# Kernel tuning notes

Hardware: AMD Instinct MI355X
Metric: run time of the kernel (lower is better)

## Reference

```python
import jax, jax.numpy as jnp
import numpy as np

B, T, D_MODEL = 2, 1024, 512
EXPAND = 2
D_INNER = D_MODEL * EXPAND
STATE = 16
K_CONV = 4


def setup_inputs() -> dict:
    key = jax.random.key(0)
    ks = jax.random.split(key, 10)
    sc = lambda k, shape: jax.random.normal(k, shape, jnp.float32) * 0.02
    return {
        "x": jax.random.normal(ks[0], (B, T, D_MODEL), jnp.float32),
        "ln_g": jnp.ones((D_MODEL,), jnp.float32),
        "ln_b": jnp.zeros((D_MODEL,), jnp.float32),
        "W_in": sc(ks[1], (2 * D_INNER, D_MODEL)),
        "conv_w": sc(ks[2], (D_INNER, 1, K_CONV)),
        "conv_b": jnp.zeros((D_INNER,), jnp.float32),
        "W_B": sc(ks[3], (STATE, D_INNER)),
        "W_C": sc(ks[4], (STATE, D_INNER)),
        "W_dt": sc(ks[5], (D_INNER, D_INNER)),
        "b_dt": jax.random.uniform(ks[6], (D_INNER,), jnp.float32, -4.0, -1.0),
        # log_A init: A_diag = -(n+1) from HiPPO, log(-A_diag) = log(n+1), broadcast over d_inner
        "log_A": jnp.broadcast_to(jnp.log(jnp.arange(1, STATE + 1, dtype=jnp.float32)), (D_INNER, STATE)),
        "W_out": sc(ks[7], (D_MODEL, D_INNER)),
    }


def _silu(v):
    return v * jax.nn.sigmoid(v)


def reference(x, ln_g, ln_b, W_in, conv_w, conv_b, W_B, W_C, W_dt, b_dt, log_A, W_out):
    residual = x
    # LayerNorm (biased variance, eps=1e-5)
    mu = x.mean(-1, keepdims=True)
    var = x.var(-1, keepdims=True)
    xn = (x - mu) * jax.lax.rsqrt(var + 1e-5) * ln_g + ln_b
    # input projection and gate split
    xz = xn @ W_in.T                      # (B,T,2*D_INNER)
    x_main, z = jnp.split(xz, 2, axis=-1)
    # depthwise causal conv1d (padding=3 then slice to T == left-pad 3)
    xc = jnp.transpose(x_main, (0, 2, 1))  # (B,D_INNER,T)
    xc = jax.lax.conv_general_dilated(
        xc, conv_w, window_strides=(1,), padding=[(K_CONV - 1, 0)],
        dimension_numbers=("NCH", "OIH", "NCH"), feature_group_count=D_INNER,
    ) + conv_b[None, :, None]
    x_main = _silu(jnp.transpose(xc, (0, 2, 1)))  # (B,T,D_INNER)
    # selective scan in fp32
    xf = x_main.astype(jnp.float32)
    Bt = xf @ W_B.T                        # (B,T,N)
    Ct = xf @ W_C.T                        # (B,T,N)
    dt = jax.nn.softplus(xf @ W_dt.T + b_dt)  # (B,T,D_INNER)
    A = -jnp.exp(log_A)                    # (D_INNER,N)
    dA = jnp.exp(A[None, None] * dt[..., None])              # (B,T,D_INNER,N)
    dBx = dt[..., None] * Bt[:, :, None, :] * xf[..., None]  # (B,T,D_INNER,N)

    def comb(c1, c2):
        a1, b1 = c1
        a2, b2 = c2
        return a1 * a2, a2 * b1 + b2

    _, h = jax.lax.associative_scan(comb, (dA, dBx), axis=1)  # h_t = dA_t*h_{t-1}+dBx_t
    y = (h * Ct[:, :, None, :]).sum(-1).astype(x.dtype)       # (B,T,D_INNER)
    out = (y * _silu(z)) @ W_out.T
    return residual + out
```

## Files before the change

kernel.cpp:

```cpp
#include <hip/hip_runtime.h>

#define T_SEQ 1024
#define DM 512
#define DI 1024
#define NS 16
#define NC 32
#define CL 32

typedef __attribute__((ext_vector_type(8))) short short8;
typedef __attribute__((ext_vector_type(4))) float f32x4;
typedef unsigned short u16;
typedef unsigned int u32;

__device__ inline float b2f(u16 u) {
    unsigned v = ((unsigned)u) << 16;
    return __builtin_bit_cast(float, v);
}
__device__ inline u16 f2b(float f) {
    unsigned u = __builtin_bit_cast(unsigned, f);
    u += 0x7fff + ((u >> 16) & 1);
    return (u16)(u >> 16);
}

__device__ inline void g2l16(const u16* g, const short* l) {
    __builtin_amdgcn_global_load_lds((const __attribute__((address_space(1))) u32*)g,
                                     (__attribute__((address_space(3))) u32*)l, 16, 0, 0);
}

template<int K> __device__ __forceinline__ void vmwait() {
    if constexpr (K == 0) asm volatile("s_waitcnt vmcnt(0)" ::: "memory");
    else if constexpr (K == 2) asm volatile("s_waitcnt vmcnt(2)" ::: "memory");
}

__global__ __launch_bounds__(256) void prep_k(const float* __restrict__ Win, const float* __restrict__ Wdt,
                       const float* __restrict__ Wout, const float* __restrict__ Wb,
                       const float* __restrict__ Wc,
                       u16* __restrict__ oWin, u16* __restrict__ wCat, u16* __restrict__ oWout,
                       const float* __restrict__ x, const float* __restrict__ g,
                       const float* __restrict__ be, u16* __restrict__ xn) {
    if (blockIdx.x < 2624) {
        int i = blockIdx.x * 256 + threadIdx.x;
        const float* s; u16* d; int off;
        if (i < 262144)      { s = Win;  d = oWin;  off = i; }
        else if (i < 524288) { s = Wdt;  d = wCat;  off = i - 262144; }
        else if (i < 655360) { s = Wout; d = oWout; off = i - 524288; }
        else if (i < 659456) { s = Wb;   d = wCat + 1048576; off = i - 655360; }
        else if (i < 663552) { s = Wc;   d = wCat + 1064960; off = i - 659456; }
        else {
            u16* dz = wCat + 1081344 + (i - 663552) * 4;
            dz[0] = 0; dz[1] = 0; dz[2] = 0; dz[3] = 0;
            return;
        }
        float4 v = ((const float4*)s)[off];
        d[off * 4 + 0] = f2b(v.x);
        d[off * 4 + 1] = f2b(v.y);
        d[off * 4 + 2] = f2b(v.z);
        d[off * 4 + 3] = f2b(v.w);
        return;
    }
    int row = blockIdx.x - 2624, tid = threadIdx.x;
    float2 v = ((const float2*)(x + row * DM))[tid];
    float s = v.x + v.y, q = v.x * v.x + v.y * v.y;
    #pragma unroll
    for (int m = 1; m < 64; m <<= 1) { s += __shfl_xor(s, m); q += __shfl_xor(q, m); }
    __shared__ float ss[4], qq[4];
    if ((tid & 63) == 0) { ss[tid >> 6] = s; qq[tid >> 6] = q; }
    __syncthreads();
    s = ss[0] + ss[1] + ss[2] + ss[3];
    q = qq[0] + qq[1] + qq[2] + qq[3];
    float mu = s / DM;
    float var = q / DM - mu * mu;
    float rs = rsqrtf(var + 1e-5f);
    int c = tid * 2;
    xn[row * DM + c]     = f2b((v.x - mu) * rs * g[c] + be[c]);
    xn[row * DM + c + 1] = f2b((v.y - mu) * rs * g[c + 1] + be[c + 1]);
}

template<int NT, int EPI>
__device__ __forceinline__ void gemm_core64(int bx, int by,
        const u16* __restrict__ A, int lda, const u16* __restrict__ Bw, int ldb,
        void* __restrict__ outp, int ldo, const float* __restrict__ extra,
        float* __restrict__ BtF, float* __restrict__ CtF) {
    __shared__ short a_sh[3 * 4096];
    __shared__ short b_sh[3 * 4096];
    int tid = threadIdx.x, w = tid >> 6, lane = tid & 63;
    int m0 = bx * 64, n0 = by * 64;
    int wr = (w >> 2) * 32, wc = (w & 3) * 16;
    int lr = lane & 15, kg = lane >> 4;
    f32x4 acc[2] = {};
    const u16* Abase = A + (size_t)m0 * lda;
    const u16* Bbase = Bw + (size_t)n0 * ldb;
    int lrow = lane >> 3;
    int cl = lane & 7;
    int row1 = w * 8 + lrow;
    int sc = cl ^ (row1 & 7);

    auto stage = [&](int buf, int kt) {
        int k0 = kt * 64;
        g2l16(Abase + (size_t)row1 * lda + k0 + sc * 8, a_sh + buf * 4096 + w * 512);
        g2l16(Bbase + (size_t)row1 * ldb + k0 + sc * 8, b_sh + buf * 4096 + w * 512);
    };

    stage(0, 0);
    stage(1, 1);
    for (int t = 0; t < NT; ++t) {
        if (t + 1 < NT) vmwait<2>();
        else vmwait<0>();
        __builtin_amdgcn_s_barrier();
        if (t + 2 < NT) stage((t + 2) % 3, t + 2);
        const short* as = a_sh + (t % 3) * 4096;
        const short* bs = b_sh + (t % 3) * 4096;
        int rsw = lr & 7;
        __builtin_amdgcn_s_setprio(1);
        #pragma unroll
        for (int kk = 0; kk < 2; ++kk) {
            short8 af[2], bfr;
            #pragma unroll
            for (int i = 0; i < 2; ++i) {
                int row = wr + i * 16 + lr;
                af[i] = *(const short8*)&as[row * 64 + ((kk * 4 + kg) ^ rsw) * 8];
            }
            {
                int row = wc + lr;
                bfr = *(const short8*)&bs[row * 64 + ((kk * 4 + kg) ^ rsw) * 8];
            }
            #pragma unroll
            for (int i = 0; i < 2; ++i)
                acc[i] = __builtin_amdgcn_mfma_f32_16x16x32_bf16(af[i], bfr, acc[i], 0, 0, 0);
        }
        __builtin_amdgcn_s_setprio(0);
    }

    int rb = (lane >> 4) * 4, cc = lane & 15;
    #pragma unroll
    for (int i = 0; i < 2; ++i) {
        #pragma unroll
        for (int r = 0; r < 4; ++r) {
            int row = m0 + wr + i * 16 + rb + r;
            int col = n0 + wc + cc;
            float v = acc[i][r];
            if (EPI == 0) {
                ((u16*)outp)[(size_t)row * ldo + col] = f2b(v);
            } else if (EPI == 2) {
                ((float*)outp)[(size_t)row * ldo + col] = v + extra[(size_t)row * ldo + col];
            } else if (EPI == 3) {
                ((float*)outp)[(size_t)row * ldo + col] = v;
            } else {
                if (col < 1024) {
                    float xx = v + extra[col];
                    float sp = (xx > 20.f) ? xx : log1pf(__expf(xx));
                    ((u16*)outp)[(size_t)row * ldo + col] = f2b(sp);
                } else if (col < 1040) {
                    BtF[(size_t)row * NS + (col - 1024)] = v;
                } else if (col < 1056) {
                    CtF[(size_t)row * NS + (col - 1040)] = v;
                }
            }
        }
    }
}

template<int NT, int EPI>
__global__ __launch_bounds__(512) void gemm8(int gx,
                                             const u16* __restrict__ A, int lda,
                                             const u16* __restrict__ Bw, int ldb,
                                             void* __restrict__ outp, int ldo,
                                             const float* __restrict__ extra,
                                             float* __restrict__ BtF, float* __restrict__ CtF) {
    int bx = blockIdx.x % gx, by = blockIdx.x / gx;
    gemm_core64<NT, EPI>(bx, by, A, lda, Bw, ldb, outp, ldo, extra, BtF, CtF);
}

__global__ __launch_bounds__(512) void gemm2_k(const u16* __restrict__ ym, const u16* __restrict__ Wout,
                                               float* __restrict__ p0, float* __restrict__ p1) {
    int bid = blockIdx.x;
    int ks = bid >> 8, rem = bid & 255;
    int bx = rem & 31, by = rem >> 5;
    float* p = ks ? p1 : p0;
    gemm_core64<8, 3>(bx, by, ym + ks * 512, DI, Wout + ks * 512, DI,
                      (void*)p, DM, nullptr, nullptr, nullptr);
}

__global__ __launch_bounds__(256) void merge_k(const float* __restrict__ p0, const float* __restrict__ p1,
                                               const float* __restrict__ x, float* __restrict__ out) {
    int i = blockIdx.x * 256 + threadIdx.x;
    float4 a = ((const float4*)p0)[i];
    float4 b = ((const float4*)p1)[i];
    float4 e = ((const float4*)x)[i];
    float4 o;
    o.x = a.x + b.x + e.x;
    o.y = a.y + b.y + e.y;
    o.z = a.z + b.z + e.z;
    o.w = a.w + b.w + e.w;
    ((float4*)out)[i] = o;
}

__global__ void conv_k(const u16* __restrict__ xz, const float* __restrict__ w,
                       const float* __restrict__ cb, u16* __restrict__ xf) {
    int idx = blockIdx.x * 256 + threadIdx.x;
    int d = idx & (DI - 1);
    int bt = idx >> 10;
    int t = bt & (T_SEQ - 1);
    float s = cb[d];
    #pragma unroll
    for (int i = 0; i < 4; ++i) {
        int tt = t - 3 + i;
        if (tt >= 0) s += w[d * 4 + i] * b2f(xz[(size_t)(bt - 3 + i) * 2048 + d]);
    }
    float sig = 1.f / (1.f + __expf(-s));
    xf[idx] = f2b(s * sig);
}

__global__ __launch_bounds__(256) void scanA(const u16* __restrict__ dt, const u16* __restrict__ xf,
                                             const float* __restrict__ Bt, const float* __restrict__ logA,
                                             float* __restrict__ Aprod, float* __restrict__ S) {
    int tid = threadIdx.x;
    int dblk = blockIdx.x & 3;
    int c = (blockIdx.x >> 2) & (NC - 1);
    int b = blockIdx.x >> 7;
    int d = dblk * 256 + tid;
    float Adn[NS], ap[NS], h[NS];
    #pragma unroll
    for (int j = 0; j < 4; ++j)
        *(float4*)&Adn[j * 4] = ((const float4*)(logA + (size_t)d * NS))[j];
    #pragma unroll
    for (int n = 0; n < NS; ++n) { Adn[n] = -__expf(Adn[n]); ap[n] = 1.f; h[n] = 0.f; }
    const u16* dtp = dt + ((size_t)b * T_SEQ + c * CL) * DI + d;
    const u16* xfp = xf + ((size_t)b * T_SEQ + c * CL) * DI + d;
    const float* Bp = Bt + ((size_t)b * T_SEQ + c * CL) * NS;
    #pragma unroll 8
    for (int i = 0; i < CL; ++i) {
        float dtv = b2f(dtp[(size_t)i * DI]);
        float xv  = b2f(xfp[(size_t)i * DI]);
        float ux = dtv * xv;
        float Bv[NS];
        #pragma unroll
        for (int j = 0; j < 4; ++j) *(float4*)&Bv[j * 4] = ((const float4*)(Bp + (size_t)i * NS))[j];
        #pragma unroll
        for (int n = 0; n < NS; ++n) {
            float dA = __expf(Adn[n] * dtv);
            h[n] = fmaf(dA, h[n], ux * Bv[n]);
            ap[n] *= dA;
        }
    }
    size_t o = ((((size_t)c * 2 + b) * DI) + d) * NS;
    #pragma unroll
    for (int j = 0; j < 4; ++j) {
        ((float4*)(Aprod + o))[j] = *(float4*)&ap[j * 4];
        ((float4*)(S + o))[j]     = *(float4*)&h[j * 4];
    }
}

__global__ __launch_bounds__(256) void scanB(const float* __restrict__ Aprod, const float* __restrict__ S,
                                             float* __restrict__ Hin) {
    int chain = blockIdx.x * 256 + threadIdx.x;
    float h = 0.f;
    #pragma unroll 8
    for (int c = 0; c < NC; ++c) {
        size_t o = (size_t)c * 32768 + chain;
        Hin[o] = h;
        h = fmaf(Aprod[o], h, S[o]);
    }
}

__global__ __launch_bounds__(256) void scanC(const u16* __restrict__ dt, const u16* __restrict__ xf,
                                             const float* __restrict__ Bt, const float* __restrict__ Ct,
                                             const float* __restrict__ logA, const float* __restrict__ Hin,
                                             const u16* __restrict__ xz, u16* __restrict__ ym) {
    int tid = threadIdx.x;
    int dblk = blockIdx.x & 3;
    int c = (blockIdx.x >> 2) & (NC - 1);
    int b = blockIdx.x >> 7;
    int d = dblk * 256 + tid;
    float Adn[NS], h[NS];
    #pragma unroll
    for (int j = 0; j < 4; ++j)
        *(float4*)&Adn[j * 4] = ((const float4*)(logA + (size_t)d * NS))[j];
    #pragma unroll
    for (int n = 0; n < NS; ++n) Adn[n] = -__expf(Adn[n]);
    size_t o = ((((size_t)c * 2 + b) * DI) + d) * NS;
    #pragma unroll
    for (int j = 0; j < 4; ++j) *(float4*)&h[j * 4] = ((const float4*)(Hin + o))[j];
    const u16* dtp = dt + ((size_t)b * T_SEQ + c * CL) * DI + d;
    const u16* xfp = xf + ((size_t)b * T_SEQ + c * CL) * DI + d;
    const float* Bp = Bt + ((size_t)b * T_SEQ + c * CL) * NS;
    const float* Cp = Ct + ((size_t)b * T_SEQ + c * CL) * NS;
    const u16* zp = xz + ((size_t)b * T_SEQ + c * CL) * 2048 + 1024 + d;
    u16* yp = ym + ((size_t)b * T_SEQ + c * CL) * DI + d;
    #pragma unroll 8
    for (int i = 0; i < CL; ++i) {
        float dtv = b2f(dtp[(size_t)i * DI]);
        float xv  = b2f(xfp[(size_t)i * DI]);
        float ux = dtv * xv;
        float Bv[NS], Cv[NS];
        #pragma unroll
        for (int j = 0; j < 4; ++j) {
            *(float4*)&Bv[j * 4] = ((const float4*)(Bp + (size_t)i * NS))[j];
            *(float4*)&Cv[j * 4] = ((const float4*)(Cp + (size_t)i * NS))[j];
        }
        float r = 0.f;
        #pragma unroll
        for (int n = 0; n < NS; ++n) {
            float dA = __expf(Adn[n] * dtv);
            h[n] = fmaf(dA, h[n], ux * Bv[n]);
            r = fmaf(h[n], Cv[n], r);
        }
        float zv = b2f(zp[(size_t)i * 2048]);
        float sz = zv / (1.f + __expf(-zv));
        yp[(size_t)i * DI] = f2b(r * sz);
    }
}

extern "C" void kernel_launch(void* const* d_in, const int* in_sizes, int n_in,
                              void* d_out, int out_size, void* d_ws, size_t ws_size,
                              hipStream_t stream) {
    const float* x     = (const float*)d_in[0];
    const float* ln_g  = (const float*)d_in[1];
    const float* ln_b  = (const float*)d_in[2];
    const float* W_in  = (const float*)d_in[3];
    const float* conv_w= (const float*)d_in[4];
    const float* conv_b= (const float*)d_in[5];
    const float* W_B   = (const float*)d_in[6];
    const float* W_C   = (const float*)d_in[7];
    const float* W_dt  = (const float*)d_in[8];
    const float* b_dt  = (const float*)d_in[9];
    const float* log_A = (const float*)d_in[10];
    const float* W_out = (const float*)d_in[11];

    char* ws = (char*)d_ws;
    u16* wInB  = (u16*)(ws + 0);
    u16* wCat  = (u16*)(ws + 2097152);
    u16* wOutB = (u16*)(ws + 4325376);
    u16* xnB   = (u16*)(ws + 5373952);
    u16* xzB   = (u16*)(ws + 7471104);
    u16* xfB   = (u16*)(ws + 15859712);
    u16* dtB   = (u16*)(ws + 20054016);
    float* BtF = (float*)(ws + 24248320);
    float* CtF = (float*)(ws + 24379392);
    u16* ymB   = (u16*)(ws + 24510464);
    float* ApF = (float*)(ws + 28704768);
    float* SF  = (float*)(ws + 32899072);
    float* HiF = (float*)(ws + 37093376);

    prep_k<<<4672, 256, 0, stream>>>(W_in, W_dt, W_out, W_B, W_C, wInB, wCat, wOutB,
                                     x, ln_g, ln_b, xnB);
    gemm8<8, 0><<<1024, 512, 0, stream>>>(32, xnB, 512, wInB, 512,
            (void*)xzB, 2048, nullptr, nullptr, nullptr);
    conv_k<<<8192, 256, 0, stream>>>(xzB, conv_w, conv_b, xfB);
    gemm8<16, 4><<<544, 512, 0, stream>>>(32, xfB, 1024, wCat, 1024,
            (void*)dtB, 1024, b_dt, BtF, CtF);
    scanA<<<256, 256, 0, stream>>>(dtB, xfB, BtF, log_A, ApF, SF);
    scanB<<<128, 256, 0, stream>>>(ApF, SF, HiF);
    scanC<<<256, 256, 0, stream>>>(dtB, xfB, BtF, CtF, log_A, HiF, xzB, ymB);
    gemm2_k<<<512, 512, 0, stream>>>(ymB, wOutB, ApF, SF);
    merge_k<<<1024, 256, 0, stream>>>(ApF, SF, x, (float*)d_out);
}
```

Before: 112.7 us.

## Fuse three scan phases into one cooperative kernel and vectorize conv

The chunked scan's three kernels (local chunk scan, cross-chunk carry propagation, final output pass) are merged into one cooperative kernel with grid-wide syncs between phases. This removes two launches and their gaps, and keeps the per-thread A values resident across phases. Separately, the depthwise conv now processes four channels per thread with vector loads and stores, cutting the grid by a factor of four. The cooperative launch needs all 256 blocks co-resident, and grid.sync has its own barrier cost.

Result: slower. 175.6 us (+55.7%).

```diff
diff --git a/kernel.cpp b/kernel.cpp
--- a/kernel.cpp
+++ b/kernel.cpp
@@ -1,4 +1,7 @@
 #include <hip/hip_runtime.h>
+#include <hip/hip_cooperative_groups.h>
+
+namespace cg = cooperative_groups;
 
 #define T_SEQ 1024
 #define DM 512
@@ -195,119 +198,134 @@
     ((float4*)out)[i] = o;
 }
 
-__global__ void conv_k(const u16* __restrict__ xz, const float* __restrict__ w,
-                       const float* __restrict__ cb, u16* __restrict__ xf) {
-    int idx = blockIdx.x * 256 + threadIdx.x;
-    int d = idx & (DI - 1);
-    int bt = idx >> 10;
+__global__ __launch_bounds__(256) void conv_k(const u16* __restrict__ xz, const float* __restrict__ w,
+                                              const float* __restrict__ cb, u16* __restrict__ xf) {
+    int base = (blockIdx.x * 256 + threadIdx.x) * 4;
+    int d0 = base & (DI - 1);
+    int bt = base >> 10;
     int t = bt & (T_SEQ - 1);
-    float s = cb[d];
+    float4 cbv = *(const float4*)(cb + d0);
+    float s0 = cbv.x, s1 = cbv.y, s2 = cbv.z, s3 = cbv.w;
+    float4 w0 = *(const float4*)(w + (d0 + 0) * 4);
+    float4 w1 = *(const float4*)(w + (d0 + 1) * 4);
+    float4 w2 = *(const float4*)(w + (d0 + 2) * 4);
+    float4 w3 = *(const float4*)(w + (d0 + 3) * 4);
+    const float* pw0 = (const float*)&w0;
+    const float* pw1 = (const float*)&w1;
+    const float* pw2 = (const float*)&w2;
+    const float* pw3 = (const float*)&w3;
     #pragma unroll
     for (int i = 0; i < 4; ++i) {
         int tt = t - 3 + i;
-        if (tt >= 0) s += w[d * 4 + i] * b2f(xz[(size_t)(bt - 3 + i) * 2048 + d]);
-    }
-    float sig = 1.f / (1.f + __expf(-s));
-    xf[idx] = f2b(s * sig);
-}
-
-__global__ __launch_bounds__(256) void scanA(const u16* __restrict__ dt, const u16* __restrict__ xf,
-                                             const float* __restrict__ Bt, const float* __restrict__ logA,
-                                             float* __restrict__ Aprod, float* __restrict__ S) {
+        if (tt >= 0) {
+            ushort4 xv = *(const ushort4*)(xz + (size_t)(bt - 3 + i) * 2048 + d0);
+            s0 += pw0[i] * b2f(xv.x);
+            s1 += pw1[i] * b2f(xv.y);
+            s2 += pw2[i] * b2f(xv.z);
+            s3 += pw3[i] * b2f(xv.w);
+        }
+    }
+    ushort4 o;
+    o.x = f2b(s0 / (1.f + __expf(-s0)));
+    o.y = f2b(s1 / (1.f + __expf(-s1)));
+    o.z = f2b(s2 / (1.f + __expf(-s2)));
+    o.w = f2b(s3 / (1.f + __expf(-s3)));
+    *(ushort4*)(xf + base) = o;
+}
+
+__global__ __launch_bounds__(256) void scan_fused(const u16* __restrict__ dt, const u16* __restrict__ xf,
+                                                  const float* __restrict__ Bt, const float* __restrict__ Ct,
+                                                  const float* __restrict__ logA, const u16* __restrict__ xz,
+                                                  u16* __restrict__ ym, float* __restrict__ Aprod,
+                                                  float* __restrict__ S, float* __restrict__ Hin) {
+    cg::grid_group grid = cg::this_grid();
     int tid = threadIdx.x;
     int dblk = blockIdx.x & 3;
     int c = (blockIdx.x >> 2) & (NC - 1);
     int b = blockIdx.x >> 7;
     int d = dblk * 256 + tid;
-    float Adn[NS], ap[NS], h[NS];
+    float Adn[NS];
     #pragma unroll
     for (int j = 0; j < 4; ++j)
         *(float4*)&Adn[j * 4] = ((const float4*)(logA + (size_t)d * NS))[j];
     #pragma unroll
-    for (int n = 0; n < NS; ++n) { Adn[n] = -__expf(Adn[n]); ap[n] = 1.f; h[n] = 0.f; }
+    for (int n = 0; n < NS; ++n) Adn[n] = -__expf(Adn[n]);
+
     const u16* dtp = dt + ((size_t)b * T_SEQ + c * CL) * DI + d;
     const u16* xfp = xf + ((size_t)b * T_SEQ + c * CL) * DI + d;
     const float* Bp = Bt + ((size_t)b * T_SEQ + c * CL) * NS;
-    #pragma unroll 8
-    for (int i = 0; i < CL; ++i) {
-        float dtv = b2f(dtp[(size_t)i * DI]);
-        float xv  = b2f(xfp[(size_t)i * DI]);
-        float ux = dtv * xv;
-        float Bv[NS];
-        #pragma unroll
-        for (int j = 0; j < 4; ++j) *(float4*)&Bv[j * 4] = ((const float4*)(Bp + (size_t)i * NS))[j];
-        #pragma unroll
-        for (int n = 0; n < NS; ++n) {
-            float dA = __expf(Adn[n] * dtv);
-            h[n] = fmaf(dA, h[n], ux * Bv[n]);
-            ap[n] *= dA;
-        }
-    }
-    size_t o = ((((size_t)c * 2 + b) * DI) + d) * NS;
-    #pragma unroll
-    for (int j = 0; j < 4; ++j) {
-        ((float4*)(Aprod + o))[j] = *(float4*)&ap[j * 4];
-        ((float4*)(S + o))[j]     = *(float4*)&h[j * 4];
-    }
-}
-
-__global__ __launch_bounds__(256) void scanB(const float* __restrict__ Aprod, const float* __restrict__ S,
-                                             float* __restrict__ Hin) {
-    int chain = blockIdx.x * 256 + threadIdx.x;
-    float h = 0.f;
-    #pragma unroll 8
-    for (int c = 0; c < NC; ++c) {
-        size_t o = (size_t)c * 32768 + chain;
-        Hin[o] = h;
-        h = fmaf(Aprod[o], h, S[o]);
-    }
-}
-
-__global__ __launch_bounds__(256) void scanC(const u16* __restrict__ dt, const u16* __restrict__ xf,
-                                             const float* __restrict__ Bt, const float* __restrict__ Ct,
-                                             const float* __restrict__ logA, const float* __restrict__ Hin,
-                                             const u16* __restrict__ xz, u16* __restrict__ ym) {
-    int tid = threadIdx.x;
-    int dblk = blockIdx.x & 3;
-    int c = (blockIdx.x >> 2) & (NC - 1);
-    int b = blockIdx.x >> 7;
-    int d = dblk * 256 + tid;
-    float Adn[NS], h[NS];
-    #pragma unroll
-    for (int j = 0; j < 4; ++j)
-        *(float4*)&Adn[j * 4] = ((const float4*)(logA + (size_t)d * NS))[j];
-    #pragma unroll
-    for (int n = 0; n < NS; ++n) Adn[n] = -__expf(Adn[n]);
-    size_t o = ((((size_t)c * 2 + b) * DI) + d) * NS;
-    #pragma unroll
-    for (int j = 0; j < 4; ++j) *(float4*)&h[j * 4] = ((const float4*)(Hin + o))[j];
-    const u16* dtp = dt + ((size_t)b * T_SEQ + c * CL) * DI + d;
-    const u16* xfp = xf + ((size_t)b * T_SEQ + c * CL) * DI + d;
-    const float* Bp = Bt + ((size_t)b * T_SEQ + c * CL) * NS;
-    const float* Cp = Ct + ((size_t)b * T_SEQ + c * CL) * NS;
-    const u16* zp = xz + ((size_t)b * T_SEQ + c * CL) * 2048 + 1024 + d;
-    u16* yp = ym + ((size_t)b * T_SEQ + c * CL) * DI + d;
-    #pragma unroll 8
-    for (int i = 0; i < CL; ++i) {
-        float dtv = b2f(dtp[(size_t)i * DI]);
-        float xv  = b2f(xfp[(size_t)i * DI]);
-        float ux = dtv * xv;
-        float Bv[NS], Cv[NS];
+    size_t oo = ((((size_t)c * 2 + b) * DI) + d) * NS;
+
+    {
+        float ap[NS], h[NS];
+        #pragma unroll
+        for (int n = 0; n < NS; ++n) { ap[n] = 1.f; h[n] = 0.f; }
+        #pragma unroll 8
+        for (int i = 0; i < CL; ++i) {
+            float dtv = b2f(dtp[(size_t)i * DI]);
+            float xv  = b2f(xfp[(size_t)i * DI]);
+            float ux = dtv * xv;
+            float Bv[NS];
+            #pragma unroll
+            for (int j = 0; j < 4; ++j) *(float4*)&Bv[j * 4] = ((const float4*)(Bp + (size_t)i * NS))[j];
+            #pragma unroll
+            for (int n = 0; n < NS; ++n) {
+                float dA = __expf(Adn[n] * dtv);
+                h[n] = fmaf(dA, h[n], ux * Bv[n]);
+                ap[n] *= dA;
+            }
+        }
         #pragma unroll
         for (int j = 0; j < 4; ++j) {
-            *(float4*)&Bv[j * 4] = ((const float4*)(Bp + (size_t)i * NS))[j];
-            *(float4*)&Cv[j * 4] = ((const float4*)(Cp + (size_t)i * NS))[j];
-        }
-        float r = 0.f;
-        #pragma unroll
-        for (int n = 0; n < NS; ++n) {
-            float dA = __expf(Adn[n] * dtv);
-            h[n] = fmaf(dA, h[n], ux * Bv[n]);
-            r = fmaf(h[n], Cv[n], r);
-        }
-        float zv = b2f(zp[(size_t)i * 2048]);
-        float sz = zv / (1.f + __expf(-zv));
-        yp[(size_t)i * DI] = f2b(r * sz);
+            ((float4*)(Aprod + oo))[j] = *(float4*)&ap[j * 4];
+            ((float4*)(S + oo))[j]     = *(float4*)&h[j * 4];
+        }
+    }
+    grid.sync();
+
+    {
+        int chain = blockIdx.x * 256 + tid;
+        if (chain < 32768) {
+            float h = 0.f;
+            #pragma unroll 8
+            for (int cc2 = 0; cc2 < NC; ++cc2) {
+                size_t o = (size_t)cc2 * 32768 + chain;
+                Hin[o] = h;
+                h = fmaf(Aprod[o], h, S[o]);
+            }
+        }
+    }
+    grid.sync();
+
+    {
+        float h[NS];
+        #pragma unroll
+        for (int j = 0; j < 4; ++j) *(float4*)&h[j * 4] = ((const float4*)(Hin + oo))[j];
+        const float* Cp = Ct + ((size_t)b * T_SEQ + c * CL) * NS;
+        const u16* zp = xz + ((size_t)b * T_SEQ + c * CL) * 2048 + 1024 + d;
+        u16* yp = ym + ((size_t)b * T_SEQ + c * CL) * DI + d;
+        #pragma unroll 8
+        for (int i = 0; i < CL; ++i) {
+            float dtv = b2f(dtp[(size_t)i * DI]);
+            float xv  = b2f(xfp[(size_t)i * DI]);
+            float ux = dtv * xv;
+            float Bv[NS], Cv[NS];
+            #pragma unroll
+            for (int j = 0; j < 4; ++j) {
+                *(float4*)&Bv[j * 4] = ((const float4*)(Bp + (size_t)i * NS))[j];
+                *(float4*)&Cv[j * 4] = ((const float4*)(Cp + (size_t)i * NS))[j];
+            }
+            float r = 0.f;
+            #pragma unroll
+            for (int n = 0; n < NS; ++n) {
+                float dA = __expf(Adn[n] * dtv);
+                h[n] = fmaf(dA, h[n], ux * Bv[n]);
+                r = fmaf(h[n], Cv[n], r);
+            }
+            float zv = b2f(zp[(size_t)i * 2048]);
+            float sz = zv / (1.f + __expf(-zv));
+            yp[(size_t)i * DI] = f2b(r * sz);
+        }
     }
 }
 
@@ -346,12 +364,17 @@
                                      x, ln_g, ln_b, xnB);
     gemm8<8, 0><<<1024, 512, 0, stream>>>(32, xnB, 512, wInB, 512,
             (void*)xzB, 2048, nullptr, nullptr, nullptr);
-    conv_k<<<8192, 256, 0, stream>>>(xzB, conv_w, conv_b, xfB);
+    conv_k<<<2048, 256, 0, stream>>>(xzB, conv_w, conv_b, xfB);
     gemm8<16, 4><<<544, 512, 0, stream>>>(32, xfB, 1024, wCat, 1024,
             (void*)dtB, 1024, b_dt, BtF, CtF);
-    scanA<<<256, 256, 0, stream>>>(dtB, xfB, BtF, log_A, ApF, SF);
-    scanB<<<128, 256, 0, stream>>>(ApF, SF, HiF);
-    scanC<<<256, 256, 0, stream>>>(dtB, xfB, BtF, CtF, log_A, HiF, xzB, ymB);
+    {
+        const u16* dt_p = dtB; const u16* xf_p = xfB;
+        const float* bt_p = BtF; const float* ct_p = CtF;
+        const float* la_p = log_A; const u16* xz_p = xzB;
+        u16* ym_p = ymB; float* ap_p = ApF; float* s_p = SF; float* hi_p = HiF;
+        void* args[] = { &dt_p, &xf_p, &bt_p, &ct_p, &la_p, &xz_p, &ym_p, &ap_p, &s_p, &hi_p };
+        hipLaunchCooperativeKernel((void*)scan_fused, dim3(256), dim3(256), args, 0, stream);
+    }
     gemm2_k<<<512, 512, 0, stream>>>(ymB, wOutB, ApF, SF);
     merge_k<<<1024, 256, 0, stream>>>(ApF, SF, x, (float*)d_out);
 }
```
